# Kernel optimization log

Hardware: AMD Instinct MI355X
Metric: run time of the kernel (lower is better)

## Reference

```python
import jax, jax.numpy as jnp
import numpy as np

B, S = 4, 2000            # meshes, nodes per mesh
N = B * S                  # total nodes
E = 32000                  # directed edges (before self loops)
H_TR, D_TR, FF, TOUT = 4, 64, 2048, 16
HID, HEADS, HC = 512, 6, 512
DEFORM_IN, NUM_LOOP = 7, 3


def setup_inputs():
    key = jax.random.key(0)
    ks = iter(jax.random.split(key, 64))
    def W(shape):
        return jax.random.normal(next(ks), shape, jnp.float32) / np.sqrt(shape[-1])
    inp = {}
    inp['conv_feat'] = jax.random.normal(next(ks), (B, 1), jnp.float32)
    inp['mesh_feat'] = jax.random.normal(next(ks), (N, 4), jnp.float32)
    inp['x'] = jax.random.normal(next(ks), (N, DEFORM_IN), jnp.float32)
    inp['edge_index'] = jax.random.randint(next(ks), (2, E), 0, N, jnp.int32)
    inp['embed_w'] = W((D_TR, 4)); inp['embed_b'] = jnp.zeros((D_TR,), jnp.float32)
    inp['in_proj_w'] = W((3 * D_TR, D_TR)); inp['in_proj_b'] = jnp.zeros((3 * D_TR,), jnp.float32)
    inp['out_proj_w'] = W((D_TR, D_TR)); inp['out_proj_b'] = jnp.zeros((D_TR,), jnp.float32)
    inp['ln1_g'] = jnp.ones((D_TR,), jnp.float32); inp['ln1_b'] = jnp.zeros((D_TR,), jnp.float32)
    inp['ln2_g'] = jnp.ones((D_TR,), jnp.float32); inp['ln2_b'] = jnp.zeros((D_TR,), jnp.float32)
    inp['ff1_w'] = W((FF, D_TR)); inp['ff1_b'] = jnp.zeros((FF,), jnp.float32)
    inp['ff2_w'] = W((D_TR, FF)); inp['ff2_b'] = jnp.zeros((D_TR,), jnp.float32)
    inp['tout_w'] = W((TOUT, D_TR)); inp['tout_b'] = jnp.zeros((TOUT,), jnp.float32)
    all_feat = DEFORM_IN - 2 + TOUT  # 21
    inp['lin_w'] = W((HID, all_feat)); inp['lin_b'] = jnp.zeros((HID,), jnp.float32)
    gin = 2 + HID  # 514
    inp['gat_wl'] = W((HEADS * HC, gin)); inp['gat_bl'] = jnp.zeros((HEADS * HC,), jnp.float32)
    inp['gat_wr'] = W((HEADS * HC, gin)); inp['gat_br'] = jnp.zeros((HEADS * HC,), jnp.float32)
    inp['gat_att'] = jax.random.normal(next(ks), (HEADS, HC), jnp.float32) / np.sqrt(HC)
    inp['gat_bias'] = jnp.zeros((HC,), jnp.float32)
    inp['coord1_w'] = W((HID // 2, HID)); inp['coord1_b'] = jnp.zeros((HID // 2,), jnp.float32)
    inp['coord2_w'] = W((2, HID // 2)); inp['coord2_b'] = jnp.zeros((2,), jnp.float32)
    return inp


def _ln(h, g, b):
    m = jnp.mean(h, -1, keepdims=True)
    v = jnp.var(h, -1, keepdims=True)
    return (h - m) / jnp.sqrt(v + 1e-5) * g + b


def _mrt_forward(conv_feat, mesh_feat, x, edge_index, embed_w, embed_b, in_proj_w, in_proj_b,
                 out_proj_w, out_proj_b, ln1_g, ln1_b, ln2_g, ln2_b, ff1_w, ff1_b, ff2_w, ff2_b,
                 tout_w, tout_b, lin_w, lin_b, gat_wl, gat_bl, gat_wr, gat_br, gat_att, gat_bias,
                 coord1_w, coord1_b, coord2_w, coord2_b):
    bsz = conv_feat.shape[0]
    feat_dim = mesh_feat.shape[-1]
    # ---- transformer encoder (1 post-norm layer, eval mode => no dropout) ----
    h = mesh_feat.reshape(bsz, -1, feat_dim) @ embed_w.T + embed_b  # [B,S,D]
    qkv = h @ in_proj_w.T + in_proj_b
    q, k, v = jnp.split(qkv, 3, axis=-1)
    dh = D_TR // H_TR
    hd = lambda t: t.reshape(bsz, -1, H_TR, dh)
    attn = jax.nn.softmax(jnp.einsum('bqhd,bkhd->bhqk', hd(q), hd(k)) / np.sqrt(dh), axis=-1)
    o = jnp.einsum('bhqk,bkhd->bqhd', attn, hd(v)).reshape(bsz, -1, D_TR)
    h = _ln(h + (o @ out_proj_w.T + out_proj_b), ln1_g, ln1_b)
    ff = jax.nn.relu(h @ ff1_w.T + ff1_b) @ ff2_w.T + ff2_b
    h = _ln(h + ff, ln2_g, ln2_b)
    feats = (h @ tout_w.T + tout_b).reshape(-1, TOUT)               # [N,16]
    feats = jnp.concatenate([x[:, 2:], feats], axis=1)             # [N,21]
    hidden = jax.nn.selu(feats @ lin_w.T + lin_b)                  # [N,512]
    # ---- recurrent GATv2 deformer loop ----
    coord = x[:, :2]
    n = x.shape[0]
    loops = jnp.arange(n, dtype=edge_index.dtype)                  # self loops (GATv2Conv default)
    src = jnp.concatenate([edge_index[0], loops])
    dst = jnp.concatenate([edge_index[1], loops])
    for _ in range(NUM_LOOP):
        inp = jnp.concatenate([coord, hidden], axis=1)             # [N,514]
        xl = (inp @ gat_wl.T + gat_bl).reshape(n, HEADS, HC)
        xr = (inp @ gat_wr.T + gat_br).reshape(n, HEADS, HC)
        e = jax.nn.leaky_relu(xl[src] + xr[dst], 0.2)              # [Etot,H,C]
        logits = jnp.einsum('ehc,hc->eh', e, gat_att)              # [Etot,H]
        mx = jax.ops.segment_max(logits, dst, num_segments=n)
        a = jnp.exp(logits - mx[dst])
        a = a / jax.ops.segment_sum(a, dst, num_segments=n)[dst]   # softmax per dst node
        agg = jax.ops.segment_sum(xl[src] * a[:, :, None], dst, num_segments=n)  # [N,H,C]
        hidden = jax.nn.selu(jnp.mean(agg, axis=1) + gat_bias)     # concat=False => head mean
        coord = jax.nn.selu(hidden @ coord1_w.T + coord1_b) @ coord2_w.T + coord2_b
    return coord


def reference(conv_feat, mesh_feat, x, edge_index, embed_w, embed_b, in_proj_w, in_proj_b,
              out_proj_w, out_proj_b, ln1_g, ln1_b, ln2_g, ln2_b, ff1_w, ff1_b, ff2_w, ff2_b,
              tout_w, tout_b, lin_w, lin_b, gat_wl, gat_bl, gat_wr, gat_br, gat_att, gat_bias,
              coord1_w, coord1_b, coord2_w, coord2_b):
    return _mrt_forward(conv_feat, mesh_feat, x, edge_index, embed_w, embed_b, in_proj_w, in_proj_b,
                        out_proj_w, out_proj_b, ln1_g, ln1_b, ln2_g, ln2_b, ff1_w, ff1_b, ff2_w, ff2_b,
                        tout_w, tout_b, lin_w, lin_b, gat_wl, gat_bl, gat_wr, gat_br, gat_att, gat_bias,
                        coord1_w, coord1_b, coord2_w, coord2_b)
```

## Files before the change

kernel.cpp:

```cpp
#include <hip/hip_runtime.h>
#include <hip/hip_bf16.h>
#include <math.h>

#define NN     8000
#define MPAD   8064
#define BATCH  4
#define SEQ    2000
#define DTR    64
#define NHTR   4
#define DHD    16
#define FFD    2048
#define TOUTD  16
#define HIDD   512
#define NHEADS 6
#define HCD    512
#define GIND   514
#define GOUT   3072
#define GOUT2  6144
#define NEDGE  32000
#define ELOOP  40000

#define K1     576
#define K2     1152

#define KSPLIT 20
#define KCH    100

#define CDIV(a,b) (((a)+(b)-1)/(b))

using bf16x8 = __attribute__((__ext_vector_type__(8))) __bf16;
using f32x4  = __attribute__((__ext_vector_type__(4))) float;

__device__ __forceinline__ float selu_f(float x){
  const float a = 1.6732632423543772848f;
  const float s = 1.0507009873554805f;
  return x > 0.f ? s * x : s * a * (__expf(x) - 1.f);
}

__device__ __forceinline__ unsigned short f2bf_rn(float x){
  unsigned u = __float_as_uint(x);
  unsigned r = (u + 0x7fffu + ((u >> 16) & 1u)) >> 16;
  return (unsigned short)r;
}
__device__ __forceinline__ float bf2f(unsigned short h){
  return __uint_as_float((unsigned)h << 16);
}

template<int ACT>
__global__ __launch_bounds__(256) void k_gemm(const float* __restrict__ A,
    const float* __restrict__ W, const float* __restrict__ bias,
    float* __restrict__ C, int M, int N, int K)
{
  __shared__ float As[16][68];
  __shared__ float Ws[16][68];
  const int tid = threadIdx.x;
  const int bm = blockIdx.y * 64, bn = blockIdx.x * 64;
  const int tx = tid & 15, ty = tid >> 4;
  float acc[4][4] = {};
  for (int k0 = 0; k0 < K; k0 += 16){
    #pragma unroll
    for (int i = 0; i < 4; ++i){
      int el = tid + (i << 8);
      int kk = el & 15, r = el >> 4;
      int gk = k0 + kk;
      int gm = bm + r;
      As[kk][r] = (gm < M && gk < K) ? A[(size_t)gm * K + gk] : 0.f;
      int gn = bn + r;
      Ws[kk][r] = (gn < N && gk < K) ? W[(size_t)gn * K + gk] : 0.f;
    }
    __syncthreads();
    #pragma unroll
    for (int kk = 0; kk < 16; ++kk){
      float av[4], wv[4];
      #pragma unroll
      for (int i = 0; i < 4; ++i) av[i] = As[kk][ty*4+i];
      #pragma unroll
      for (int j = 0; j < 4; ++j) wv[j] = Ws[kk][tx*4+j];
      #pragma unroll
      for (int i = 0; i < 4; ++i)
        #pragma unroll
        for (int j = 0; j < 4; ++j) acc[i][j] = fmaf(av[i], wv[j], acc[i][j]);
    }
    __syncthreads();
  }
  #pragma unroll
  for (int i = 0; i < 4; ++i){
    int gm = bm + ty*4 + i;
    if (gm >= M) continue;
    #pragma unroll
    for (int j = 0; j < 4; ++j){
      int gn = bn + tx*4 + j;
      if (gn >= N) continue;
      float v = acc[i][j] + bias[gn];
      if (ACT == 1) v = fmaxf(v, 0.f);
      if (ACT == 2) v = selu_f(v);
      C[(size_t)gm * N + gn] = v;
    }
  }
}

__global__ __launch_bounds__(256) void k_gemm_sk(const float* __restrict__ A,
    const float* __restrict__ W, float* __restrict__ part,
    int M, int N, int K, int kchunk)
{
  __shared__ float As[16][68];
  __shared__ float Ws[16][68];
  const int tid = threadIdx.x;
  const int bm = blockIdx.y * 64, bn = blockIdx.x * 64;
  const int kbeg = blockIdx.z * kchunk;
  const int tx = tid & 15, ty = tid >> 4;
  float acc[4][4] = {};
  for (int k0 = kbeg; k0 < kbeg + kchunk; k0 += 16){
    #pragma unroll
    for (int i = 0; i < 4; ++i){
      int el = tid + (i << 8);
      int kk = el & 15, r = el >> 4;
      int gk = k0 + kk;
      int gm = bm + r;
      As[kk][r] = (gm < M && gk < K) ? A[(size_t)gm * K + gk] : 0.f;
      int gn = bn + r;
      Ws[kk][r] = (gn < N && gk < K) ? W[(size_t)gn * K + gk] : 0.f;
    }
    __syncthreads();
    #pragma unroll
    for (int kk = 0; kk < 16; ++kk){
      float av[4], wv[4];
      #pragma unroll
      for (int i = 0; i < 4; ++i) av[i] = As[kk][ty*4+i];
      #pragma unroll
      for (int j = 0; j < 4; ++j) wv[j] = Ws[kk][tx*4+j];
      #pragma unroll
      for (int i = 0; i < 4; ++i)
        #pragma unroll
        for (int j = 0; j < 4; ++j) acc[i][j] = fmaf(av[i], wv[j], acc[i][j]);
    }
    __syncthreads();
  }
  float* pz = part + (size_t)blockIdx.z * M * N;
  #pragma unroll
  for (int i = 0; i < 4; ++i){
    int gm = bm + ty*4 + i;
    if (gm >= M) continue;
    #pragma unroll
    for (int j = 0; j < 4; ++j){
      int gn = bn + tx*4 + j;
      if (gn >= N) continue;
      pz[(size_t)gm * N + gn] = acc[i][j];
    }
  }
}

__global__ __launch_bounds__(256) void k_addln8(const float* __restrict__ x,
    const float* __restrict__ part, const float* __restrict__ bias,
    const float* __restrict__ g, const float* __restrict__ b,
    float* __restrict__ out)
{
  int row = blockIdx.x * 4 + (threadIdx.x >> 6);
  int lane = threadIdx.x & 63;
  if (row >= NN) return;
  float y = bias[lane];
  #pragma unroll
  for (int z = 0; z < 8; ++z) y += part[(size_t)z*NN*DTR + (size_t)row*64 + lane];
  float v = x[(size_t)row*64 + lane] + y;
  float s1 = v, s2 = v * v;
  #pragma unroll
  for (int o = 32; o; o >>= 1){ s1 += __shfl_xor(s1, o); s2 += __shfl_xor(s2, o); }
  float mean = s1 * (1.f/64.f);
  float var  = s2 * (1.f/64.f) - mean * mean;
  float r = rsqrtf(var + 1e-5f);
  out[(size_t)row*64 + lane] = (v - mean) * r * g[lane] + b[lane];
}

__global__ __launch_bounds__(256) void k_coord(const float* __restrict__ part,
    const float* __restrict__ c1b, const float* __restrict__ w2,
    const float* __restrict__ b2, float* __restrict__ out,
    short* __restrict__ abf)
{
  int n = blockIdx.x, t = threadIdx.x;
  float v = c1b[t];
  #pragma unroll
  for (int z = 0; z < 4; ++z) v += part[(size_t)z*NN*256 + (size_t)n*256 + t];
  v = selu_f(v);
  float d0 = v * w2[t], d1 = v * w2[256 + t];
  #pragma unroll
  for (int o = 32; o; o >>= 1){ d0 += __shfl_xor(d0, o); d1 += __shfl_xor(d1, o); }
  __shared__ float red[8];
  int wv = t >> 6;
  if ((t & 63) == 0){ red[wv] = d0; red[4 + wv] = d1; }
  __syncthreads();
  if (t < 2){
    float c = (t == 0 ? red[0]+red[1]+red[2]+red[3] + b2[0]
                      : red[4]+red[5]+red[6]+red[7] + b2[1]);
    out[(size_t)n*2 + t] = c;
    abf[(size_t)n*K2 + t] = (short)f2bf_rn(c);
  }
}

__global__ void k_cvt_w(const float* __restrict__ W, short* __restrict__ Wbf)
{
  int i = blockIdx.x * blockDim.x + threadIdx.x;
  if (i >= GOUT * K1) return;
  int n = i / K1, k = i - K1 * n;
  float v = (k < GIND) ? W[(size_t)n * GIND + k] : 0.f;
  Wbf[i] = (short)f2bf_rn(v);
}

__global__ void k_cvt_a(const float* __restrict__ coord,
                        const float* __restrict__ hidden,
                        short* __restrict__ Abf)
{
  int i = blockIdx.x * blockDim.x + threadIdx.x;
  if (i >= MPAD * K1) return;
  int n = i / K1, k = i - K1 * n;
  float v = 0.f;
  if (n < NN && k < GIND)
    v = (k < 2) ? coord[(size_t)n*2 + k] : hidden[(size_t)n*HIDD + k - 2];
  Abf[(size_t)n * K2 + k] = (short)f2bf_rn(v);
}

__global__ void k_wfuse(const float* __restrict__ ipw, const float* __restrict__ ipb,
                        const float* __restrict__ ew, const float* __restrict__ eb,
                        float* __restrict__ Wp, float* __restrict__ bp)
{
  int c = blockIdx.x * blockDim.x + threadIdx.x;
  if (c >= 192) return;
  float w4[4] = {0.f, 0.f, 0.f, 0.f};
  float bb = 0.f;
  for (int d = 0; d < 64; ++d){
    float wq = ipw[c*64 + d];
    #pragma unroll
    for (int j = 0; j < 4; ++j) w4[j] = fmaf(wq, ew[d*4 + j], w4[j]);
    bb = fmaf(wq, eb[d], bb);
  }
  #pragma unroll
  for (int j = 0; j < 4; ++j) Wp[c*4 + j] = w4[j];
  bp[c] = bb + ipb[c];
}

__global__ __launch_bounds__(256) void k_embqkv(const float* __restrict__ mesh,
    const float* __restrict__ ew, const float* __restrict__ eb,
    const float* __restrict__ Wp, const float* __restrict__ bp,
    float* __restrict__ h, float* __restrict__ qkv)
{
  int n = blockIdx.x, t = threadIdx.x;
  float m0 = mesh[n*4+0], m1 = mesh[n*4+1], m2 = mesh[n*4+2], m3 = mesh[n*4+3];
  if (t < 64){
    const float* wr = ew + t*4;
    h[(size_t)n*64 + t] =
      fmaf(m0, wr[0], fmaf(m1, wr[1], fmaf(m2, wr[2], m3*wr[3]))) + eb[t];
  } else {
    int c = t - 64;
    const float* wr = Wp + c*4;
    qkv[(size_t)n*192 + c] =
      fmaf(m0, wr[0], fmaf(m1, wr[1], fmaf(m2, wr[2], m3*wr[3]))) + bp[c];
  }
}

__global__ __launch_bounds__(256) void k_gat_mfma(
    const short* __restrict__ Abf, const short* __restrict__ Wbf,
    const float* __restrict__ bl, const float* __restrict__ br,
    unsigned short* __restrict__ Cb)
{
  __shared__ __align__(16) short smem[2 * 128 * 64];
  short* As = smem;
  short* Bs = smem + 128 * 64;
  const int tid  = threadIdx.x;
  int lin = blockIdx.y * 48 + blockIdx.x;
  int xcd = lin & 7;
  int idx = lin >> 3;
  int nb  = xcd * 6 + idx % 6;
  int mb  = idx / 6;
  const int bm = mb * 128, bn = nb * 128;
  const int w    = tid >> 6, lane = tid & 63;
  const int wr   = w >> 1, wc = w & 1;
  const int lrow = lane & 15;

  f32x4 acc[4][4];
  #pragma unroll
  for (int i = 0; i < 4; ++i)
    #pragma unroll
    for (int j = 0; j < 4; ++j) acc[i][j] = (f32x4){0.f, 0.f, 0.f, 0.f};

  for (int kt = 0; kt < 9; ++kt){
    int koff = kt * 64;
    __syncthreads();
    #pragma unroll
    for (int i = 0; i < 4; ++i){
      int l  = i * 256 + tid;
      int r  = l >> 3, j = l & 7;
      int js = j ^ (r & 7);
      const short* ga = Abf + (size_t)(bm + r) * K2 + koff + js * 8;
      const short* gb = Wbf + (size_t)(bn + r) * K1 + koff + js * 8;
      short* la = As + ((i * 256 + w * 64) << 3);
      short* lb = Bs + ((i * 256 + w * 64) << 3);
      __builtin_amdgcn_global_load_lds(
          (const __attribute__((address_space(1))) unsigned*)ga,
          (__attribute__((address_space(3))) unsigned*)la, 16, 0, 0);
      __builtin_amdgcn_global_load_lds(
          (const __attribute__((address_space(1))) unsigned*)gb,
          (__attribute__((address_space(3))) unsigned*)lb, 16, 0, 0);
    }
    __syncthreads();
    #pragma unroll
    for (int ks = 0; ks < 2; ++ks){
      const int co = ((ks * 4 + (lane >> 4)) ^ (lrow & 7)) * 8;
      bf16x8 fa[4], fb[4];
      #pragma unroll
      for (int mi = 0; mi < 4; ++mi)
        fa[mi] = *(const bf16x8*)&As[(wr*64 + mi*16 + lrow) * 64 + co];
      #pragma unroll
      for (int ni = 0; ni < 4; ++ni)
        fb[ni] = *(const bf16x8*)&Bs[(wc*64 + ni*16 + lrow) * 64 + co];
      #pragma unroll
      for (int mi = 0; mi < 4; ++mi)
        #pragma unroll
        for (int ni = 0; ni < 4; ++ni)
          acc[mi][ni] = __builtin_amdgcn_mfma_f32_16x16x32_bf16(
              fa[mi], fb[ni], acc[mi][ni], 0, 0, 0);
    }
  }
  __syncthreads();
  unsigned short* Ct = (unsigned short*)smem;
  #pragma unroll
  for (int mi = 0; mi < 4; ++mi){
    #pragma unroll
    for (int ni = 0; ni < 4; ++ni){
      int col = wc*64 + ni*16 + lrow;
      int gn  = bn + col;
      float bv = (gn < GOUT) ? bl[gn] : br[gn - GOUT];
      #pragma unroll
      for (int j = 0; j < 4; ++j){
        int row  = wr*64 + mi*16 + (lane >> 4)*4 + j;
        int colp = col ^ (((row >> 2) & 3) << 4);
        Ct[row*128 + colp] = f2bf_rn(acc[mi][ni][j] + bv);
      }
    }
  }
  __syncthreads();
  #pragma unroll
  for (int c = 0; c < 8; ++c){
    int g   = c*256 + tid;
    int row = g >> 4, cc = g & 15;
    int ccp = cc ^ (((row >> 2) & 3) << 1);
    int gm  = bm + row;
    if (gm < NN){
      bf16x8 v = *(const bf16x8*)&Ct[row*128 + ccp*8];
      *(bf16x8*)&Cb[(size_t)gm * GOUT2 + bn + cc*8] = v;
    }
  }
}

__global__ __launch_bounds__(128) void k_attn_part(const float* __restrict__ qkv,
    float* __restrict__ Pm, float* __restrict__ Pl, float* __restrict__ Pacc)
{
  __shared__ float Ks[KCH][DHD];
  __shared__ float Vs[KCH][DHD];
  const int q1 = blockIdx.x * 128 + threadIdx.x;
  const int q2 = q1 + 1024;
  const int bh = blockIdx.y;
  const int b  = bh >> 2, h = bh & 3;
  const int ks = blockIdx.z;
  const bool v2 = q2 < SEQ;
  const float SC = 0.25f * 1.4426950408889634f;
  float qv1[DHD], qv2[DHD];
  {
    const float4* qr = (const float4*)(qkv + ((size_t)(b*SEQ + q1))*192 + h*DHD);
    #pragma unroll
    for (int j = 0; j < 4; ++j){
      float4 t = qr[j];
      qv1[j*4+0] = t.x; qv1[j*4+1] = t.y; qv1[j*4+2] = t.z; qv1[j*4+3] = t.w;
    }
  }
  if (v2){
    const float4* qr = (const float4*)(qkv + ((size_t)(b*SEQ + q2))*192 + h*DHD);
    #pragma unroll
    for (int j = 0; j < 4; ++j){
      float4 t = qr[j];
      qv2[j*4+0] = t.x; qv2[j*4+1] = t.y; qv2[j*4+2] = t.z; qv2[j*4+3] = t.w;
    }
  } else {
    #pragma unroll
    for (int j = 0; j < DHD; ++j) qv2[j] = 0.f;
  }
  const int kbeg = ks * KCH;
  for (int el = threadIdx.x; el < KCH * 4; el += 128){
    int r = el >> 2, d4 = el & 3;
    const float4* base = (const float4*)(qkv + ((size_t)(b*SEQ + kbeg + r))*192 + h*DHD);
    ((float4*)Ks[r])[d4] = base[16 + d4];
    ((float4*)Vs[r])[d4] = base[32 + d4];
  }
  __syncthreads();
  float m1 = -1e30f, l1 = 0.f, a1[DHD] = {};
  float m2 = -1e30f, l2 = 0.f, a2[DHD] = {};
  for (int r = 0; r < KCH; ++r){
    float s1 = 0.f, s2 = 0.f;
    #pragma unroll
    for (int d = 0; d < DHD; ++d){
      float kd = Ks[r][d];
      s1 = fmaf(qv1[d], kd, s1);
      s2 = fmaf(qv2[d], kd, s2);
    }
    s1 *= SC; s2 *= SC;
    if (__any((s1 > m1 + 8.f) || (s2 > m2 + 8.f))){
      float mn1 = fmaxf(m1, s1), mn2 = fmaxf(m2, s2);
      float c1 = exp2f(m1 - mn1), c2 = exp2f(m2 - mn2);
      l1 *= c1; l2 *= c2;
      #pragma unroll
      for (int d = 0; d < DHD; ++d){ a1[d] *= c1; a2[d] *= c2; }
      m1 = mn1; m2 = mn2;
    }
    float p1 = exp2f(s1 - m1), p2 = exp2f(s2 - m2);
    l1 += p1; l2 += p2;
    #pragma unroll
    for (int d = 0; d < DHD; ++d){
      float vd = Vs[r][d];
      a1[d] = fmaf(p1, vd, a1[d]);
      a2[d] = fmaf(p2, vd, a2[d]);
    }
  }
  {
    size_t qi = ((size_t)bh * SEQ + q1) * KSPLIT + ks;
    Pm[qi] = m1; Pl[qi] = l1;
    #pragma unroll
    for (int d = 0; d < DHD; ++d) Pacc[qi*DHD + d] = a1[d];
  }
  if (v2){
    size_t qi = ((size_t)bh * SEQ + q2) * KSPLIT + ks;
    Pm[qi] = m2; Pl[qi] = l2;
    #pragma unroll
    for (int d = 0; d < DHD; ++d) Pacc[qi*DHD + d] = a2[d];
  }
}

__global__ void k_attn_comb(const float* __restrict__ Pm, const float* __restrict__ Pl,
                            const float* __restrict__ Pacc, float* __restrict__ o)
{
  int qi = blockIdx.x * blockDim.x + threadIdx.x;
  if (qi >= BATCH * NHTR * SEQ) return;
  float m = -1e30f;
  #pragma unroll
  for (int ks = 0; ks < KSPLIT; ++ks) m = fmaxf(m, Pm[(size_t)qi*KSPLIT + ks]);
  float l = 0.f, acc[DHD] = {};
  #pragma unroll
  for (int ks = 0; ks < KSPLIT; ++ks){
    size_t p = (size_t)qi*KSPLIT + ks;
    float sc = exp2f(Pm[p] - m);
    l += Pl[p] * sc;
    #pragma unroll
    for (int d = 0; d < DHD; ++d) acc[d] = fmaf(Pacc[p*DHD + d], sc, acc[d]);
  }
  int bh = qi / SEQ, q = qi - bh * SEQ;
  int b = bh >> 2, h = bh & 3;
  float inv = 1.f / l;
  #pragma unroll
  for (int d = 0; d < DHD; ++d)
    o[((size_t)(b*SEQ + q))*64 + h*DHD + d] = acc[d] * inv;
}

__global__ __launch_bounds__(256) void k_addln(const float* __restrict__ x,
    const float* __restrict__ y, const float* __restrict__ g,
    const float* __restrict__ b, float* __restrict__ out)
{
  int row = blockIdx.x * 4 + (threadIdx.x >> 6);
  int lane = threadIdx.x & 63;
  if (row >= NN) return;
  float v = x[(size_t)row*64 + lane] + y[(size_t)row*64 + lane];
  float s1 = v, s2 = v * v;
  #pragma unroll
  for (int o = 32; o; o >>= 1){ s1 += __shfl_xor(s1, o); s2 += __shfl_xor(s2, o); }
  float mean = s1 * (1.f/64.f);
  float var  = s2 * (1.f/64.f) - mean * mean;
  float r = rsqrtf(var + 1e-5f);
  out[(size_t)row*64 + lane] = (v - mean) * r * g[lane] + b[lane];
}

__global__ void k_prep(const float* __restrict__ x, const float* __restrict__ tout,
                       float* __restrict__ feats, float* __restrict__ coord)
{
  int i = blockIdx.x * blockDim.x + threadIdx.x;
  if (i >= NN * 23) return;
  int n = i / 23, c = i - 23*n;
  if (c < 21)
    feats[(size_t)n*21 + c] = (c < 5) ? x[(size_t)n*7 + 2 + c] : tout[(size_t)n*16 + c - 5];
  else
    coord[(size_t)n*2 + (c - 21)] = x[(size_t)n*7 + (c - 21)];
}

__global__ void k_count(const int* __restrict__ dst, int* __restrict__ cnt)
{
  int e = blockIdx.x * blockDim.x + threadIdx.x;
  if (e >= ELOOP) return;
  int d = (e < NEDGE) ? dst[e] : e - NEDGE;
  atomicAdd(&cnt[d], 1);
}

__global__ __launch_bounds__(1024) void k_scan(const int* __restrict__ cnt,
                                               int* __restrict__ ptr)
{
  __shared__ int part[1024];
  int tid = threadIdx.x;
  const int per = 8;
  int loc[per]; int s = 0;
  int base = tid * per;
  #pragma unroll
  for (int i = 0; i < per; ++i){
    int v = (base + i < NN) ? cnt[base + i] : 0;
    loc[i] = s; s += v;
  }
  part[tid] = s;
  __syncthreads();
  for (int off = 1; off < 1024; off <<= 1){
    int v = 0;
    if (tid >= off) v = part[tid - off];
    __syncthreads();
    if (tid >= off) part[tid] += v;
    __syncthreads();
  }
  int pre = tid ? part[tid - 1] : 0;
  #pragma unroll
  for (int i = 0; i < per; ++i)
    if (base + i < NN) ptr[base + i] = pre + loc[i];
  if (tid == 1023) ptr[NN] = part[1023];
}

__global__ void k_fill(const int* __restrict__ dst, const int* __restrict__ ptr,
                       int* __restrict__ fil, int* __restrict__ eid)
{
  int e = blockIdx.x * blockDim.x + threadIdx.x;
  if (e >= ELOOP) return;
  int d = (e < NEDGE) ? dst[e] : e - NEDGE;
  int pos = ptr[d] + atomicAdd(&fil[d], 1);
  eid[pos] = e;
}

__global__ __launch_bounds__(256) void k_logits(const unsigned short* __restrict__ xc,
    const int* __restrict__ src_a, const int* __restrict__ dst_a,
    const int* __restrict__ eid, const float* __restrict__ att,
    float* __restrict__ logits2)
{
  int bid = blockIdx.x;
  int wgs = (bid & 7) * 1250 + (bid >> 3);
  int pos = wgs * 4 + (threadIdx.x >> 6);
  if (pos >= ELOOP) return;
  int lane = threadIdx.x & 63;
  int e = eid[pos];
  int s = (e < NEDGE) ? src_a[e] : e - NEDGE;
  int d = (e < NEDGE) ? dst_a[e] : e - NEDGE;
  const uint4* pl = (const uint4*)(xc + (size_t)s * GOUT2);
  const uint4* pr = (const uint4*)(xc + (size_t)d * GOUT2 + GOUT);
  const float4* pa = (const float4*)att;
  #pragma unroll 2
  for (int h = 0; h < NHEADS; ++h){
    uint4 ua = pl[h*64 + lane];
    uint4 ub = pr[h*64 + lane];
    float4 w0 = pa[h*128 + lane*2], w1 = pa[h*128 + lane*2 + 1];
    float acc = 0.f;
    auto pair = [&](unsigned a, unsigned b, float wl, float wh){
      float vl = __uint_as_float(a << 16)        + __uint_as_float(b << 16);
      float vh = __uint_as_float(a & 0xffff0000u)+ __uint_as_float(b & 0xffff0000u);
      vl = vl > 0.f ? vl : 0.2f * vl;
      vh = vh > 0.f ? vh : 0.2f * vh;
      acc = fmaf(vl, wl, acc);
      acc = fmaf(vh, wh, acc);
    };
    pair(ua.x, ub.x, w0.x, w0.y);
    pair(ua.y, ub.y, w0.z, w0.w);
    pair(ua.z, ub.z, w1.x, w1.y);
    pair(ua.w, ub.w, w1.z, w1.w);
    #pragma unroll
    for (int o2 = 32; o2; o2 >>= 1) acc += __shfl_xor(acc, o2);
    if (lane == 0) logits2[pos*NHEADS + h] = acc;
  }
}

__global__ void k_stats(const float* __restrict__ logits2, const int* __restrict__ ptr,
                        float* __restrict__ mx, float* __restrict__ inv)
{
  int i = blockIdx.x * blockDim.x + threadIdx.x;
  if (i >= NN * NHEADS) return;
  int n = i / NHEADS, h = i - NHEADS * n;
  int s0 = ptr[n], s1 = ptr[n + 1];
  float m = -1e30f;
  for (int t = s0; t < s1; ++t) m = fmaxf(m, logits2[t*NHEADS + h]);
  float s = 0.f;
  for (int t = s0; t < s1; ++t) s += __expf(logits2[t*NHEADS + h] - m);
  mx[i] = m; inv[i] = 1.f / s;
}

__global__ __launch_bounds__(256) void k_agg(const unsigned short* __restrict__ xc,
    const float* __restrict__ logits2, const float* __restrict__ mx,
    const float* __restrict__ inv, const int* __restrict__ ptr,
    const int* __restrict__ eid, const int* __restrict__ src_a,
    const float* __restrict__ gbias, float* __restrict__ hidden,
    short* __restrict__ abf)
{
  const int n = blockIdx.x;
  const int tid = threadIdx.x;
  __shared__ float a_sh[64 * NHEADS];
  __shared__ int src_sh[64];
  const int s0 = ptr[n];
  const int deg = ptr[n + 1] - s0;
  float acc[12] = {};
  for (int base = 0; base < deg; base += 64){
    int cnt = min(64, deg - base);
    __syncthreads();
    for (int t = tid; t < cnt * NHEADS; t += 256){
      int ei = t / NHEADS, h = t - NHEADS * ei;
      a_sh[t] = __expf(logits2[(s0 + base + ei)*NHEADS + h] - mx[n*NHEADS + h])
                * inv[n*NHEADS + h];
      if (h == 0){
        int e = eid[s0 + base + ei];
        src_sh[ei] = (e < NEDGE) ? src_a[e] : e - NEDGE;
      }
    }
    __syncthreads();
    for (int i2 = 0; i2 < cnt; ++i2){
      const unsigned* row = (const unsigned*)(xc + (size_t)src_sh[i2] * GOUT2);
      #pragma unroll
      for (int k = 0; k < NHEADS; ++k){
        unsigned u = row[tid + (k << 8)];
        float wgt = a_sh[i2*NHEADS + k];
        acc[2*k]   = fmaf(__uint_as_float(u << 16),         wgt, acc[2*k]);
        acc[2*k+1] = fmaf(__uint_as_float(u & 0xffff0000u), wgt, acc[2*k+1]);
      }
    }
  }
  float m0 = (acc[0]+acc[2]+acc[4]+acc[6]+acc[8]+acc[10]) * (1.f/6.f);
  float m1 = (acc[1]+acc[3]+acc[5]+acc[7]+acc[9]+acc[11]) * (1.f/6.f);
  float2 out;
  out.x = selu_f(m0 + gbias[2*tid]);
  out.y = selu_f(m1 + gbias[2*tid + 1]);
  *(float2*)&hidden[(size_t)n*HIDD + 2*tid] = out;
  unsigned short h0 = f2bf_rn(out.x), h1 = f2bf_rn(out.y);
  *(unsigned*)&abf[(size_t)n*K2 + 2 + 2*tid] = (unsigned)h0 | ((unsigned)h1 << 16);
}

extern "C" void kernel_launch(void* const* d_in, const int* in_sizes, int n_in,
                              void* d_out, int out_size, void* d_ws, size_t ws_size,
                              hipStream_t stream)
{
  const float* mesh     = (const float*)d_in[1];
  const float* xin      = (const float*)d_in[2];
  const int*   ei       = (const int*)d_in[3];
  const float* embed_w  = (const float*)d_in[4];
  const float* embed_b  = (const float*)d_in[5];
  const float* in_proj_w= (const float*)d_in[6];
  const float* in_proj_b= (const float*)d_in[7];
  const float* out_proj_w=(const float*)d_in[8];
  const float* out_proj_b=(const float*)d_in[9];
  const float* ln1_g    = (const float*)d_in[10];
  const float* ln1_b    = (const float*)d_in[11];
  const float* ln2_g    = (const float*)d_in[12];
  const float* ln2_b    = (const float*)d_in[13];
  const float* ff1_w    = (const float*)d_in[14];
  const float* ff1_b    = (const float*)d_in[15];
  const float* ff2_w    = (const float*)d_in[16];
  const float* ff2_b    = (const float*)d_in[17];
  const float* tout_w   = (const float*)d_in[18];
  const float* tout_b   = (const float*)d_in[19];
  const float* lin_w    = (const float*)d_in[20];
  const float* lin_b    = (const float*)d_in[21];
  const float* gat_wl   = (const float*)d_in[22];
  const float* gat_bl   = (const float*)d_in[23];
  const float* gat_wr   = (const float*)d_in[24];
  const float* gat_br   = (const float*)d_in[25];
  const float* gat_att  = (const float*)d_in[26];
  const float* gat_bias = (const float*)d_in[27];
  const float* coord1_w = (const float*)d_in[28];
  const float* coord1_b = (const float*)d_in[29];
  const float* coord2_w = (const float*)d_in[30];
  const float* coord2_b = (const float*)d_in[31];

  const int* esrc = ei;
  const int* edst = ei + NEDGE;

  char* ws = (char*)d_ws;
  size_t off = 0;
  auto alloc = [&](size_t nbytes){
    size_t o = off; off += (nbytes + 255) & ~(size_t)255; return o;
  };
  float* hidden = (float*)(ws + alloc((size_t)NN * HIDD * 4));
  float* coord  = (float*)(ws + alloc((size_t)NN * 2 * 4));
  unsigned short* xc = (unsigned short*)(ws + alloc((size_t)NN * GOUT2 * 2));
  float* logits = (float*)(ws + alloc((size_t)ELOOP * NHEADS * 4));
  float* mxb    = (float*)(ws + alloc((size_t)NN * NHEADS * 4));
  float* invb   = (float*)(ws + alloc((size_t)NN * NHEADS * 4));
  int*   ptr    = (int*)(ws + alloc((size_t)(NN + 1) * 4));
  int*   eid    = (int*)(ws + alloc((size_t)ELOOP * 4));
  int*   cnt    = (int*)(ws + alloc((size_t)NN * 4));
  int*   fil    = (int*)(ws + alloc((size_t)NN * 4));
  short* abf    = (short*)(ws + alloc((size_t)MPAD * K2 * 2));
  short* wlbf   = (short*)(ws + alloc((size_t)GOUT * K1 * 2));
  short* wrbf   = (short*)(ws + alloc((size_t)GOUT * K1 * 2));
  float* part_c1= (float*)(ws + alloc((size_t)4 * NN * 256 * 4));
  float* Wp     = (float*)(ws + alloc((size_t)192 * 4 * 4));
  float* bp     = (float*)(ws + alloc((size_t)192 * 4));

  char* arena = (char*)xc;
  float* h       = (float*)(arena + ((size_t)0  << 20));
  float* o       = (float*)(arena + ((size_t)2  << 20));
  float* tmp     = (float*)(arena + ((size_t)4  << 20));
  float* feats   = (float*)(arena + ((size_t)6  << 20));
  float* toutb   = (float*)(arena + ((size_t)7  << 20));
  float* qkv     = (float*)(arena + ((size_t)8  << 20));
  float* Pm      = (float*)(arena + ((size_t)15 << 20));
  float* Pl      = (float*)(arena + ((size_t)18 << 20));
  float* Pacc    = (float*)(arena + ((size_t)21 << 20));
  float* part_f2 = (float*)(arena + ((size_t)8  << 20));
  float* ffmid   = (float*)(arena + ((size_t)28 << 20));

  k_wfuse<<<1, 192, 0, stream>>>(in_proj_w, in_proj_b, embed_w, embed_b, Wp, bp);
  k_embqkv<<<NN, 256, 0, stream>>>(mesh, embed_w, embed_b, Wp, bp, h, qkv);
  k_attn_part<<<dim3(CDIV(SEQ,256), BATCH*NHTR, KSPLIT), 128, 0, stream>>>(qkv, Pm, Pl, Pacc);
  k_attn_comb<<<CDIV(BATCH*NHTR*SEQ, 256), 256, 0, stream>>>(Pm, Pl, Pacc, o);
  k_gemm<0><<<dim3(1, CDIV(NN,64)), 256, 0, stream>>>(o, out_proj_w, out_proj_b, tmp, NN, 64, 64);
  k_addln<<<CDIV(NN,4), 256, 0, stream>>>(h, tmp, ln1_g, ln1_b, h);
  k_gemm<1><<<dim3(CDIV(FFD,64), CDIV(NN,64)), 256, 0, stream>>>(h, ff1_w, ff1_b, ffmid, NN, FFD, DTR);
  k_gemm_sk<<<dim3(1, CDIV(NN,64), 8), 256, 0, stream>>>(ffmid, ff2_w, part_f2, NN, DTR, FFD, 256);
  k_addln8<<<CDIV(NN,4), 256, 0, stream>>>(h, part_f2, ff2_b, ln2_g, ln2_b, h);
  k_gemm<0><<<dim3(1, CDIV(NN,64)), 256, 0, stream>>>(h, tout_w, tout_b, toutb, NN, TOUTD, DTR);
  k_prep<<<CDIV(NN*23, 256), 256, 0, stream>>>(xin, toutb, feats, coord);
  k_gemm<2><<<dim3(CDIV(HIDD,64), CDIV(NN,64)), 256, 0, stream>>>(feats, lin_w, lin_b, hidden, NN, HIDD, 21);

  hipMemsetAsync(cnt, 0, (size_t)NN * 4, stream);
  hipMemsetAsync(fil, 0, (size_t)NN * 4, stream);
  k_count<<<CDIV(ELOOP, 256), 256, 0, stream>>>(edst, cnt);
  k_scan<<<1, 1024, 0, stream>>>(cnt, ptr);
  k_fill<<<CDIV(ELOOP, 256), 256, 0, stream>>>(edst, ptr, fil, eid);
  k_cvt_w<<<CDIV(GOUT*K1, 256), 256, 0, stream>>>(gat_wl, wlbf);
  k_cvt_w<<<CDIV(GOUT*K1, 256), 256, 0, stream>>>(gat_wr, wrbf);
  k_cvt_a<<<CDIV(MPAD*K1, 256), 256, 0, stream>>>(coord, hidden, abf);

  for (int it = 0; it < 3; ++it){
    k_gat_mfma<<<dim3(48, 63), 256, 0, stream>>>(abf, wlbf, gat_bl, gat_br, xc);
    k_logits<<<ELOOP/4, 256, 0, stream>>>(xc, esrc, edst, eid, gat_att, logits);
    k_stats<<<CDIV(NN*NHEADS, 256), 256, 0, stream>>>(logits, ptr, mxb, invb);
    k_agg<<<NN, 256, 0, stream>>>(xc, logits, mxb, invb, ptr, eid, esrc, gat_bias, hidden, abf);
    k_gemm_sk<<<dim3(CDIV(256,64), CDIV(NN,64), 4), 256, 0, stream>>>(hidden, coord1_w, part_c1, NN, 256, HIDD, 128);
    float* cdst = (it == 2) ? (float*)d_out : coord;
    k_coord<<<NN, 256, 0, stream>>>(part_c1, coord1_b, coord2_w, coord2_b, cdst, abf);
  }
}
```

Measured before the change: 968.7 us.

## Compute coord1 layer with bf16 MFMA GEMM reusing the bf16 activation buffer

Replaces the fp32 split-K coord1 GEMM plus partial-sum reduction with a bf16 MFMA kernel that reads the already-converted bf16 hidden buffer (abf) and a padded bf16 copy of coord1_w, fusing bias and SELU into the epilogue. k_coord shrinks to reading the finished activation. This removes the fp32 GEMM and the four-way partial buffer traffic, at the cost of bf16 rounding of the hidden activations and weights in this layer. It relies on k_agg writing abf for hidden before the call, and on the first two K columns of abf (coord) being masked by zero weights.

```diff
diff --git a/kernel.cpp b/kernel.cpp
--- a/kernel.cpp
+++ b/kernel.cpp
@@ -171,16 +171,12 @@
   out[(size_t)row*64 + lane] = (v - mean) * r * g[lane] + b[lane];
 }
 
-__global__ __launch_bounds__(256) void k_coord(const float* __restrict__ part,
-    const float* __restrict__ c1b, const float* __restrict__ w2,
-    const float* __restrict__ b2, float* __restrict__ out,
-    short* __restrict__ abf)
+__global__ __launch_bounds__(256) void k_coord2(const float* __restrict__ c1,
+    const float* __restrict__ w2, const float* __restrict__ b2,
+    float* __restrict__ out, short* __restrict__ abf)
 {
   int n = blockIdx.x, t = threadIdx.x;
-  float v = c1b[t];
-  #pragma unroll
-  for (int z = 0; z < 4; ++z) v += part[(size_t)z*NN*256 + (size_t)n*256 + t];
-  v = selu_f(v);
+  float v = c1[(size_t)n*256 + t];
   float d0 = v * w2[t], d1 = v * w2[256 + t];
   #pragma unroll
   for (int o = 32; o; o >>= 1){ d0 += __shfl_xor(d0, o); d1 += __shfl_xor(d1, o); }
@@ -202,6 +198,15 @@
   if (i >= GOUT * K1) return;
   int n = i / K1, k = i - K1 * n;
   float v = (k < GIND) ? W[(size_t)n * GIND + k] : 0.f;
+  Wbf[i] = (short)f2bf_rn(v);
+}
+
+__global__ void k_cvt_wc(const float* __restrict__ W, short* __restrict__ Wbf)
+{
+  int i = blockIdx.x * blockDim.x + threadIdx.x;
+  if (i >= 256 * K1) return;
+  int n = i / K1, k = i - K1 * n;
+  float v = (k >= 2 && k < GIND) ? W[(size_t)n * HIDD + (k - 2)] : 0.f;
   Wbf[i] = (short)f2bf_rn(v);
 }
 
@@ -346,6 +351,79 @@
     if (gm < NN){
       bf16x8 v = *(const bf16x8*)&Ct[row*128 + ccp*8];
       *(bf16x8*)&Cb[(size_t)gm * GOUT2 + bn + cc*8] = v;
+    }
+  }
+}
+
+__global__ __launch_bounds__(256) void k_c1_mfma(
+    const short* __restrict__ Abf, const short* __restrict__ Wbf,
+    const float* __restrict__ c1b, float* __restrict__ C)
+{
+  __shared__ __align__(16) short smem[2 * 128 * 64];
+  short* As = smem;
+  short* Bs = smem + 128 * 64;
+  const int tid  = threadIdx.x;
+  const int bm = blockIdx.y * 128, bn = blockIdx.x * 128;
+  const int w    = tid >> 6, lane = tid & 63;
+  const int wr   = w >> 1, wc = w & 1;
+  const int lrow = lane & 15;
+
+  f32x4 acc[4][4];
+  #pragma unroll
+  for (int i = 0; i < 4; ++i)
+    #pragma unroll
+    for (int j = 0; j < 4; ++j) acc[i][j] = (f32x4){0.f, 0.f, 0.f, 0.f};
+
+  for (int kt = 0; kt < 9; ++kt){
+    int koff = kt * 64;
+    __syncthreads();
+    #pragma unroll
+    for (int i = 0; i < 4; ++i){
+      int l  = i * 256 + tid;
+      int r  = l >> 3, j = l & 7;
+      int js = j ^ (r & 7);
+      const short* ga = Abf + (size_t)(bm + r) * K2 + koff + js * 8;
+      const short* gb = Wbf + (size_t)(bn + r) * K1 + koff + js * 8;
+      short* la = As + ((i * 256 + w * 64) << 3);
+      short* lb = Bs + ((i * 256 + w * 64) << 3);
+      __builtin_amdgcn_global_load_lds(
+          (const __attribute__((address_space(1))) unsigned*)ga,
+          (__attribute__((address_space(3))) unsigned*)la, 16, 0, 0);
+      __builtin_amdgcn_global_load_lds(
+          (const __attribute__((address_space(1))) unsigned*)gb,
+          (__attribute__((address_space(3))) unsigned*)lb, 16, 0, 0);
+    }
+    __syncthreads();
+    #pragma unroll
+    for (int ks = 0; ks < 2; ++ks){
+      const int co = ((ks * 4 + (lane >> 4)) ^ (lrow & 7)) * 8;
+      bf16x8 fa[4], fb[4];
+      #pragma unroll
+      for (int mi = 0; mi < 4; ++mi)
+        fa[mi] = *(const bf16x8*)&As[(wr*64 + mi*16 + lrow) * 64 + co];
+      #pragma unroll
+      for (int ni = 0; ni < 4; ++ni)
+        fb[ni] = *(const bf16x8*)&Bs[(wc*64 + ni*16 + lrow) * 64 + co];
+      #pragma unroll
+      for (int mi = 0; mi < 4; ++mi)
+        #pragma unroll
+        for (int ni = 0; ni < 4; ++ni)
+          acc[mi][ni] = __builtin_amdgcn_mfma_f32_16x16x32_bf16(
+              fa[mi], fb[ni], acc[mi][ni], 0, 0, 0);
+    }
+  }
+  #pragma unroll
+  for (int mi = 0; mi < 4; ++mi){
+    #pragma unroll
+    for (int ni = 0; ni < 4; ++ni){
+      int gn = bn + wc*64 + ni*16 + lrow;
+      float bv = c1b[gn];
+      #pragma unroll
+      for (int j = 0; j < 4; ++j){
+        int gm = bm + wr*64 + mi*16 + (lane >> 4) * 4 + j;
+        if (gm < NN)
+          C[(size_t)gm * 256 + gn] = selu_f(acc[mi][ni][j] + bv);
+      }
     }
   }
 }
@@ -692,7 +770,8 @@
   short* abf    = (short*)(ws + alloc((size_t)MPAD * K2 * 2));
   short* wlbf   = (short*)(ws + alloc((size_t)GOUT * K1 * 2));
   short* wrbf   = (short*)(ws + alloc((size_t)GOUT * K1 * 2));
-  float* part_c1= (float*)(ws + alloc((size_t)4 * NN * 256 * 4));
+  short* wcb    = (short*)(ws + alloc((size_t)256 * K1 * 2));
+  float* c1     = (float*)(ws + alloc((size_t)NN * 256 * 4));
   float* Wp     = (float*)(ws + alloc((size_t)192 * 4 * 4));
   float* bp     = (float*)(ws + alloc((size_t)192 * 4));
 
@@ -729,6 +808,7 @@
   k_fill<<<CDIV(ELOOP, 256), 256, 0, stream>>>(edst, ptr, fil, eid);
   k_cvt_w<<<CDIV(GOUT*K1, 256), 256, 0, stream>>>(gat_wl, wlbf);
   k_cvt_w<<<CDIV(GOUT*K1, 256), 256, 0, stream>>>(gat_wr, wrbf);
+  k_cvt_wc<<<CDIV(256*K1, 256), 256, 0, stream>>>(coord1_w, wcb);
   k_cvt_a<<<CDIV(MPAD*K1, 256), 256, 0, stream>>>(coord, hidden, abf);
 
   for (int it = 0; it < 3; ++it){
@@ -736,8 +816,8 @@
     k_logits<<<ELOOP/4, 256, 0, stream>>>(xc, esrc, edst, eid, gat_att, logits);
     k_stats<<<CDIV(NN*NHEADS, 256), 256, 0, stream>>>(logits, ptr, mxb, invb);
     k_agg<<<NN, 256, 0, stream>>>(xc, logits, mxb, invb, ptr, eid, esrc, gat_bias, hidden, abf);
-    k_gemm_sk<<<dim3(CDIV(256,64), CDIV(NN,64), 4), 256, 0, stream>>>(hidden, coord1_w, part_c1, NN, 256, HIDD, 128);
+    k_c1_mfma<<<dim3(2, 63), 256, 0, stream>>>(abf, wcb, coord1_b, c1);
     float* cdst = (it == 2) ? (float*)d_out : coord;
-    k_coord<<<NN, 256, 0, stream>>>(part_c1, coord1_b, coord2_w, coord2_b, cdst, abf);
-  }
-}
+    k_coord2<<<NN, 256, 0, stream>>>(c1, coord2_w, coord2_b, cdst, abf);
+  }
+}
```

Measured after the change: 869.7 us. 1.11x faster.
